# Optimization experiments

Measured on AMD Instinct MI355X. Metric: run time of the kernel, lower is better.

The kernel has to match this reference:

```python
import jax, jax.numpy as jnp
import numpy as np

VAR0, VAR1 = 0.1, 0.2
CONF_THR = 0.02
NMS_THR = 0.4
PRE_K = 5000
POST_K = 750
N = 85680


def setup_inputs() -> dict:
    key = jax.random.key(0)
    k0, k1, k2, k3 = jax.random.split(key, 4)
    return {
        "loc": jax.random.normal(k0, (N, 4), jnp.float32),
        "conf": jax.random.uniform(k1, (N, 2), jnp.float32),
        "landmarks": jax.random.normal(k2, (N, 10), jnp.float32),
        "priors": jax.random.uniform(k3, (N, 4), jnp.float32),
        "img_w": 1920,
        "img_h": 1088,
    }


def _decode_boxes(loc, priors):
    # center-size decode -> xyxy
    cxy = priors[:, :2] + loc[:, :2] * VAR0 * priors[:, 2:]
    wh = priors[:, 2:] * jnp.exp(loc[:, 2:] * VAR1)
    return jnp.concatenate([cxy - wh * 0.5, cxy + wh * 0.5], axis=-1)


def _decode_landmarks(lmk, priors):
    pts = lmk.reshape(-1, 5, 2)                       # [N,5,2]
    out = priors[:, None, :2] + pts * VAR0 * priors[:, None, 2:]
    return out.reshape(-1, 10)


def _pairwise_iou(boxes):
    # boxes: [K,4] xyxy
    area = (boxes[:, 2] - boxes[:, 0]) * (boxes[:, 3] - boxes[:, 1])
    lt = jnp.maximum(boxes[:, None, :2], boxes[None, :, :2])  # [K,K,2]
    rb = jnp.minimum(boxes[:, None, 2:], boxes[None, :, 2:])
    wh = jnp.clip(rb - lt, 0.0)
    inter = wh[..., 0] * wh[..., 1]
    union = area[:, None] + area[None, :] - inter
    return inter / jnp.maximum(union, 1e-12)


def _greedy_nms(boxes, valid, thr):
    # boxes already sorted by descending score; valid marks real candidates.
    K = boxes.shape[0]
    iou = _pairwise_iou(boxes)                         # [K,K]
    idx = jnp.arange(K)

    def body(i, keep):
        suppress = keep[i] & (iou[i] > thr) & (idx > i)
        return keep & ~suppress

    return jax.lax.fori_loop(0, K, body, valid)


def reference(loc, conf, landmarks, priors, img_w, img_h):
    w = jnp.float32(img_w)
    h = jnp.float32(img_h)
    bbox_scale = jnp.array([w, h, w, h], jnp.float32)
    lmk_scale = jnp.tile(jnp.array([w, h], jnp.float32), 5)

    boxes = _decode_boxes(loc, priors) * bbox_scale          # [N,4]
    lmk = _decode_landmarks(landmarks, priors) * lmk_scale   # [N,10]
    scores = conf[:, 1]                                      # [N]

    # confidence filter fused into top-k via -inf masking (static shapes)
    masked = jnp.where(scores > CONF_THR, scores, -jnp.inf)
    top_scores, order = jax.lax.top_k(masked, PRE_K)         # [PRE_K]
    boxes_k = boxes[order]
    lmk_k = lmk[order]
    valid_k = top_scores > CONF_THR

    keep = _greedy_nms(boxes_k, valid_k, NMS_THR)            # [PRE_K] bool

    # compact kept rows (already score-sorted) into fixed [POST_K,15]
    rank = jnp.cumsum(keep) - 1
    rows = jnp.concatenate([boxes_k, top_scores[:, None], lmk_k], axis=1)
    dest = jnp.where(keep & (rank < POST_K), rank, POST_K)   # OOB -> dropped
    out = jnp.zeros((POST_K, 15), jnp.float32).at[dest].set(rows, mode="drop")
    return out
```

## Files before the change

kernel.cpp:

```cpp
#include <hip/hip_runtime.h>
#include <hip/hip_bf16.h>
#include <math.h>

#define N_IN 85680
#define PRE_K 5000
#define POST_K 750
#define NW 79
#define NPAD 5056
#define HSIZE 8192
#define CAND_MAX 8192
#define CONF_THR 0.02f
#define NMS_THR 0.4f
#define BITS_THR 0x3CA3D70Bu
#define NGRP 20
#define ZBYTES 66624

typedef unsigned int u32;
typedef unsigned long long u64;

__device__ __forceinline__ int cbase(int k) { return k * (5088 - 32 * k); }

__device__ __forceinline__ float opaquef(float x) { asm volatile("" : "+v"(x)); return x; }

__device__ __forceinline__ u32 bucket_of(u32 bits) {
    u32 b = (bits - BITS_THR) >> 13;
    return b >= HSIZE ? (HSIZE - 1) : b;
}

__global__ __launch_bounds__(256) void zero_kernel(u32* __restrict__ p) {
    int i = blockIdx.x * 256 + threadIdx.x;
    if (i < ZBYTES / 4) p[i] = 0u;
}

__global__ __launch_bounds__(256) void hist_kernel(const float2* __restrict__ conf2,
                                                   u32* __restrict__ hist) {
    __shared__ u32 h[HSIZE];
    for (int b = threadIdx.x; b < HSIZE; b += 256) h[b] = 0u;
    __syncthreads();
    int i = blockIdx.x * 256 + threadIdx.x;
    if (i < N_IN) {
        float s = conf2[i].y;
        if (s > CONF_THR) atomicAdd(&h[bucket_of(__float_as_uint(s))], 1u);
    }
    __syncthreads();
    for (int b = threadIdx.x; b < HSIZE; b += 256) {
        u32 v = h[b];
        if (v) atomicAdd(&hist[b], v);
    }
}

__global__ __launch_bounds__(1024) void scan_kernel(const u32* __restrict__ hist,
                                                    u32* __restrict__ bsel,
                                                    u32* __restrict__ bstart) {
    __shared__ u32 tot[1024];
    int c = threadIdx.x;
    u32 lh[8];
    u32 t = 0;
#pragma unroll
    for (int k = 0; k < 8; ++k) { lh[k] = hist[c * 8 + k]; t += lh[k]; }
    tot[c] = t;
    __syncthreads();
    for (int d = 1; d < 1024; d <<= 1) {
        u32 v = tot[c] + ((c + d < 1024) ? tot[c + d] : 0u);
        __syncthreads();
        tot[c] = v;
        __syncthreads();
    }
    u32 above = (c + 1 < 1024) ? tot[c + 1] : 0u;
    u32 s = above;
    for (int k = 7; k >= 0; --k) { bstart[c * 8 + k] = s; s += lh[k]; }
    if (above < PRE_K && above + t >= PRE_K) {
        u32 cum = above;
        for (int k = 7; k >= 0; --k) {
            cum += lh[k];
            if (cum >= PRE_K) { bsel[0] = (u32)(c * 8 + k); break; }
        }
    }
    if (c == 0 && tot[0] < PRE_K) bsel[0] = 0u;
}

__global__ __launch_bounds__(256) void compact_kernel(const float2* __restrict__ conf2,
                                                      const u32* __restrict__ bsel,
                                                      const u32* __restrict__ bstart,
                                                      u32* __restrict__ bfill,
                                                      u64* __restrict__ cand) {
    int i = blockIdx.x * 256 + threadIdx.x;
    if (i >= N_IN) return;
    float sc = conf2[i].y;
    if (!(sc > CONF_THR)) return;
    u32 bits = __float_as_uint(sc);
    u32 b = bucket_of(bits);
    if (b < bsel[0]) return;
    u32 pos = bstart[b] + atomicAdd(&bfill[b], 1u);
    if (pos < CAND_MAX) cand[pos] = ((u64)bits << 32) | (u64)(u32)(~(u32)i);
}

__global__ __launch_bounds__(256) void rankdec_kernel(const u64* __restrict__ cand,
                                                      const u32* __restrict__ bstart,
                                                      const u32* __restrict__ bfill,
                                                      const u32* __restrict__ bsel,
                                                      const float4* __restrict__ loc4,
                                                      const float4* __restrict__ pri4,
                                                      const float* __restrict__ lmk,
                                                      const int* __restrict__ imw,
                                                      const int* __restrict__ imh,
                                                      float4* __restrict__ rows4,
                                                      float4* __restrict__ boxes,
                                                      u64* __restrict__ validm) {
    u32 bs = bsel[0];
    u32 total = bstart[bs] + bfill[bs];
    if (total > CAND_MAX) total = CAND_MAX;
    float W = (float)(*imw), H = (float)(*imh);
    for (u32 s = blockIdx.x * blockDim.x + threadIdx.x; s < total;
         s += gridDim.x * blockDim.x) {
        u64 key = cand[s];
        u32 b = bucket_of((u32)(key >> 32));
        u32 st = bstart[b];
        u32 en = st + bfill[b];
        if (en > CAND_MAX) en = CAND_MAX;
        u32 r = st;
        for (u32 j = st; j < en; ++j) r += (cand[j] > key) ? 1u : 0u;
        if (r >= PRE_K) continue;
        u32 i = ~(u32)key;
        float score = __uint_as_float((u32)(key >> 32));
        float4 L = loc4[i];
        float4 P = pri4[i];
        float cx = P.x + opaquef((L.x * 0.1f) * P.z);
        float cy = P.y + opaquef((L.y * 0.1f) * P.w);
        float bw = P.z * (float)exp((double)(L.z * 0.2f));
        float bh = P.w * (float)exp((double)(L.w * 0.2f));
        float hw = opaquef(bw * 0.5f), hh = opaquef(bh * 0.5f);
        float x0 = (cx - hw) * W, y0 = (cy - hh) * H;
        float x1 = (cx + hw) * W, y1 = (cy + hh) * H;
        boxes[r] = make_float4(x0, y0, x1, y1);
        float lm[10];
#pragma unroll
        for (int p = 0; p < 5; ++p) {
            float2 q = ((const float2*)lmk)[(size_t)i * 5 + p];
            lm[2 * p]     = (P.x + opaquef((q.x * 0.1f) * P.z)) * W;
            lm[2 * p + 1] = (P.y + opaquef((q.y * 0.1f) * P.w)) * H;
        }
        float4* row = rows4 + (size_t)r * 4;
        row[0] = make_float4(x0, y0, x1, y1);
        row[1] = make_float4(score, lm[0], lm[1], lm[2]);
        row[2] = make_float4(lm[3], lm[4], lm[5], lm[6]);
        row[3] = make_float4(lm[7], lm[8], lm[9], 0.f);
        atomicOr(&validm[r >> 6], 1ull << (r & 63));
    }
}

__global__ __launch_bounds__(256) void mask_kernel(const float4* __restrict__ boxes,
                                                   u64* __restrict__ cmask) {
    __shared__ float4 cb4[4][64];
    int wv = threadIdx.x >> 6, t = threadIdx.x & 63;
    int t64 = blockIdx.x * 4 + wv;
    if (t64 >= NW * (NW + 1) / 2) return;
    int rc = (int)((sqrtf(8.0f * (float)t64 + 1.0f) - 1.0f) * 0.5f);
    while ((rc + 1) * (rc + 2) / 2 <= t64) ++rc;
    while (rc * (rc + 1) / 2 > t64) --rc;
    int cc = t64 - rc * (rc + 1) / 2;
    cb4[wv][t] = boxes[cc * 64 + t];
    int i = rc * 64 + t;
    float4 bi = boxes[i];
    float areai = (bi.z - bi.x) * (bi.w - bi.y);
    u64 word = 0ull;
#pragma unroll 4
    for (int k = 0; k < 64; ++k) {
        float4 bj = cb4[wv][k];
        float areaj = (bj.z - bj.x) * (bj.w - bj.y);
        float ltx = fmaxf(bi.x, bj.x), lty = fmaxf(bi.y, bj.y);
        float rbx = fminf(bi.z, bj.z), rby = fminf(bi.w, bj.w);
        float wx = fmaxf(rbx - ltx, 0.f), wy = fmaxf(rby - lty, 0.f);
        float inter = opaquef(wx * wy);
        float uni = fmaxf(areai + areaj - inter, 1e-12f);
        float iou = inter / uni;
        if (iou > NMS_THR) word |= (1ull << k);
    }
    if (i < PRE_K) cmask[(size_t)(cbase(cc) + (i - 64 * cc))] = word;
}

#define FC(k, q) cmask[(size_t)(cbase(k) + (q) - 64 * (k))]

#define LDC(j, r, d) ((((d) + (j)) < w0) ? FC((d) + (j), q##r) : 0ull)

#define WAITG(need)                                                                   \
    for (;;) {                                                                        \
        u32 d_ = __hip_atomic_load(&doneCnt, __ATOMIC_RELAXED,                        \
                                   __HIP_MEMORY_SCOPE_WORKGROUP);                     \
        if (d_ > (u32)NGRP) { dead = true; break; }                                   \
        if (d_ >= (u32)(need)) break;                                                 \
    }                                                                                 \
    asm volatile("" ::: "memory");

__device__ __forceinline__ u64 nms_solve(u64 valw, u64 sup, u64 dlow) {
    u64 keep = valw & ~__ballot(sup != 0ull);
    for (;;) {
        u64 conm = __ballot((dlow & keep) != 0ull);
        u64 cm = conm & keep;
        if (cm == 0ull) break;
        u64 U = keep & ~conm;
        u64 rem = __ballot((dlow & U) != 0ull) & keep;
        keep &= ~rem;
    }
    return keep;
}

__global__ __launch_bounds__(512) void reduce_scatter_kernel(const u64* __restrict__ cmask,
                                                             const u64* __restrict__ validm,
                                                             const float* __restrict__ rows,
                                                             float* __restrict__ out) {
    int tid = threadIdx.x;
    int g = tid >> 6, lane = tid & 63;
    __shared__ u64 keepAll[96];
    __shared__ u32 totG[32];
    __shared__ u32 doneCnt;
    __shared__ u32 wpref[97];
    for (int k = tid; k < 96; k += 512) keepAll[k] = 0ull;
    if (tid == 0) doneCnt = 0u;
    __syncthreads();
    u64 lmask = (1ull << lane) - 1ull;

    for (int s = 0; s < 3; ++s) {
        int G = s * 8 + g;
        if (G >= NGRP) break;
        int w0 = 4 * G;
        int nwg = NW - w0; if (nwg > 4) nwg = 4;
        int q0 = 64 * w0 + lane;
        int q1 = q0 + 64;
        int q2 = q0 + 128;
        int q3 = (nwg > 3) ? (q0 + 192) : q0;
        u64 t00 = FC(w0, q0);
        u64 t10 = (nwg > 1) ? FC(w0, q1) : 0ull;
        u64 t11 = (nwg > 1) ? FC(w0 + 1, q1) : 0ull;
        u64 t20 = (nwg > 2) ? FC(w0, q2) : 0ull;
        u64 t21 = (nwg > 2) ? FC(w0 + 1, q2) : 0ull;
        u64 t22 = (nwg > 2) ? FC(w0 + 2, q2) : 0ull;
        u64 t30 = (nwg > 3) ? FC(w0, q3) : 0ull;
        u64 t31 = (nwg > 3) ? FC(w0 + 1, q3) : 0ull;
        u64 t32 = (nwg > 3) ? FC(w0 + 2, q3) : 0ull;
        u64 t33 = (nwg > 3) ? FC(w0 + 3, q3) : 0ull;
        u64 v0 = validm[w0];
        u64 v1 = (nwg > 1) ? validm[w0 + 1] : 0ull;
        u64 v2 = (nwg > 2) ? validm[w0 + 2] : 0ull;
        u64 v3 = (nwg > 3) ? validm[w0 + 3] : 0ull;
        u64 sup0 = 0, sup1 = 0, sup2 = 0, sup3 = 0;
        bool dead = false;

        int d0 = 0;
        u64 a00=0,a01=0,a02=0,a03=0, a10=0,a11=0,a12=0,a13=0,
            a20=0,a21=0,a22=0,a23=0, a30=0,a31=0,a32=0,a33=0;
        if (w0 > 0) {
            a00=LDC(0,0,0); a01=LDC(0,1,0); a02=LDC(0,2,0); a03=LDC(0,3,0);
            a10=LDC(1,0,0); a11=LDC(1,1,0); a12=LDC(1,2,0); a13=LDC(1,3,0);
            a20=LDC(2,0,0); a21=LDC(2,1,0); a22=LDC(2,2,0); a23=LDC(2,3,0);
            a30=LDC(3,0,0); a31=LDC(3,1,0); a32=LDC(3,2,0); a33=LDC(3,3,0);
        }
        asm volatile("" ::: "memory");
        while (d0 < w0) {
            int d1 = d0 + 4;
            u64 b00=0,b01=0,b02=0,b03=0, b10=0,b11=0,b12=0,b13=0,
                b20=0,b21=0,b22=0,b23=0, b30=0,b31=0,b32=0,b33=0;
            if (d1 < w0) {
                b00=LDC(0,0,d1); b01=LDC(0,1,d1); b02=LDC(0,2,d1); b03=LDC(0,3,d1);
                b10=LDC(1,0,d1); b11=LDC(1,1,d1); b12=LDC(1,2,d1); b13=LDC(1,3,d1);
                b20=LDC(2,0,d1); b21=LDC(2,1,d1); b22=LDC(2,2,d1); b23=LDC(2,3,d1);
                b30=LDC(3,0,d1); b31=LDC(3,1,d1); b32=LDC(3,2,d1); b33=LDC(3,3,d1);
            }
            asm volatile("" ::: "memory");
            WAITG((d0 >> 2) + 1)
            if (dead) break;
            u64 ka = keepAll[d0],     kb = keepAll[d0 + 1];
            u64 kc = keepAll[d0 + 2], kd = keepAll[d0 + 3];
            sup0 |= ((ka & a00) | (kb & a10)) | ((kc & a20) | (kd & a30));
            sup1 |= ((ka & a01) | (kb & a11)) | ((kc & a21) | (kd & a31));
            sup2 |= ((ka & a02) | (kb & a12)) | ((kc & a22) | (kd & a32));
            sup3 |= ((ka & a03) | (kb & a13)) | ((kc & a23) | (kd & a33));
            a00=b00;a01=b01;a02=b02;a03=b03; a10=b10;a11=b11;a12=b12;a13=b13;
            a20=b20;a21=b21;a22=b22;a23=b23; a30=b30;a31=b31;a32=b32;a33=b33;
            d0 = d1;
        }
        if (!dead) {
            __builtin_amdgcn_s_setprio(1);
            u32 tp = (G > 0) ? totG[G - 1] : 0u;
            u64 k0 = 0, k1 = 0, k2 = 0, k3 = 0;
            if (tp < POST_K) {
                k0 = nms_solve(v0, sup0, t00 & lmask);
                sup1 |= k0 & t10; sup2 |= k0 & t20; sup3 |= k0 & t30;
                k1 = nms_solve(v1, sup1, t11 & lmask);
                sup2 |= k1 & t21; sup3 |= k1 & t31;
                k2 = nms_solve(v2, sup2, t22 & lmask);
                sup3 |= k2 & t32;
                k3 = nms_solve(v3, sup3, t33 & lmask);
            }
            if (lane == 0) {
                keepAll[w0]     = k0;
                keepAll[w0 + 1] = k1;
                keepAll[w0 + 2] = k2;
                keepAll[w0 + 3] = k3;
                u32 tk = tp + (u32)(__popcll(k0) + __popcll(k1) + __popcll(k2) + __popcll(k3));
                totG[G] = tk;
                asm volatile("s_waitcnt lgkmcnt(0)" ::: "memory");
                __hip_atomic_store(&doneCnt,
                                   (tk >= POST_K) ? (u32)(NGRP + 9) : (u32)(G + 1),
                                   __ATOMIC_RELAXED, __HIP_MEMORY_SCOPE_WORKGROUP);
            }
            __builtin_amdgcn_s_setprio(0);
        } else {
            break;
        }
    }
    __syncthreads();

    if (tid == 0) {
        u32 s = 0;
        for (int w = 0; w < NW; ++w) { wpref[w] = s; s += (u32)__popcll(keepAll[w]); }
        wpref[NW] = s;
    }
    __syncthreads();
    u32 totk = wpref[NW]; if (totk > POST_K) totk = POST_K;
    for (int r = tid; r < PRE_K; r += 512) {
        int w = r >> 6, b = r & 63;
        u64 kw = keepAll[w];
        if ((kw >> b) & 1ull) {
            u32 rank = wpref[w] + (u32)__popcll(kw & ((1ull << b) - 1ull));
            if (rank < POST_K) {
                const float* src = rows + (size_t)r * 16;
                float* dst = out + (size_t)rank * 15;
#pragma unroll
                for (int c2 = 0; c2 < 15; ++c2) dst[c2] = src[c2];
            }
        }
    }
    for (int r = (int)totk + tid; r < POST_K; r += 512) {
        float* dst = out + (size_t)r * 15;
#pragma unroll
        for (int c2 = 0; c2 < 15; ++c2) dst[c2] = 0.f;
    }
}

extern "C" void kernel_launch(void* const* d_in, const int* in_sizes, int n_in,
                              void* d_out, int out_size, void* d_ws, size_t ws_size,
                              hipStream_t stream) {
    const float* loc = (const float*)d_in[0];
    const float2* conf2 = (const float2*)d_in[1];
    const float* lmk = (const float*)d_in[2];
    const float* pri = (const float*)d_in[3];
    const int* imw = (const int*)d_in[4];
    const int* imh = (const int*)d_in[5];
    float* out = (float*)d_out;
    char* base = (char*)d_ws;

    u32* hist   = (u32*)(base + 0);
    u32* bfill  = (u32*)(base + 32768);
    u32* bsel   = (u32*)(base + 65536);
    u64* validm = (u64*)(base + 65600);
    u32* bstart = (u32*)(base + 67648);
    u64* cand   = (u64*)(base + 100416);
    float* rows = (float*)(base + 165952);
    float4* boxes = (float4*)(base + 485952);
    u64* cmask  = (u64*)(base + 566848);

    zero_kernel<<<(ZBYTES / 4 + 255) / 256, 256, 0, stream>>>((u32*)base);

    hist_kernel<<<(N_IN + 255) / 256, 256, 0, stream>>>(conf2, hist);
    scan_kernel<<<1, 1024, 0, stream>>>(hist, bsel, bstart);
    compact_kernel<<<(N_IN + 255) / 256, 256, 0, stream>>>(conf2, bsel, bstart, bfill, cand);
    rankdec_kernel<<<48, 256, 0, stream>>>(cand, bstart, bfill, bsel, (const float4*)loc,
                                           (const float4*)pri, lmk, imw, imh,
                                           (float4*)rows, boxes, validm);
    mask_kernel<<<(NW * (NW + 1) / 2 + 3) / 4, 256, 0, stream>>>(boxes, cmask);
    reduce_scatter_kernel<<<1, 512, 0, stream>>>(cmask, validm, rows, out);
}
```

Before: 93.44 us.

## Fuse histogram scan and candidate compaction into one kernel with a spin-wait flag

The single-block scan kernel and the compaction kernel are merged into one launch. Block 0 computes the bucket prefix sums and threshold bucket over 256 threads with 32 buckets each, then publishes a release flag. The other blocks preload their scores and spin on an acquire load until the flag is set. This removes one kernel launch boundary and overlaps the score loads with the scan. The cost is spin-waiting blocks and reliance on block 0 being scheduled, which is a forward-progress assumption.

```diff
diff --git a/kernel.cpp b/kernel.cpp
--- a/kernel.cpp
+++ b/kernel.cpp
@@ -49,45 +49,54 @@
     }
 }
 
-__global__ __launch_bounds__(1024) void scan_kernel(const u32* __restrict__ hist,
-                                                    u32* __restrict__ bsel,
-                                                    u32* __restrict__ bstart) {
-    __shared__ u32 tot[1024];
+__global__ __launch_bounds__(256) void scancompact_kernel(const float2* __restrict__ conf2,
+                                                          const u32* __restrict__ hist,
+                                                          u32* __restrict__ bsel,
+                                                          u32* __restrict__ bstart,
+                                                          u32* __restrict__ bfill,
+                                                          u32* __restrict__ flag,
+                                                          u64* __restrict__ cand) {
     int c = threadIdx.x;
-    u32 lh[8];
-    u32 t = 0;
-#pragma unroll
-    for (int k = 0; k < 8; ++k) { lh[k] = hist[c * 8 + k]; t += lh[k]; }
-    tot[c] = t;
-    __syncthreads();
-    for (int d = 1; d < 1024; d <<= 1) {
-        u32 v = tot[c] + ((c + d < 1024) ? tot[c + d] : 0u);
+    if (blockIdx.x == 0) {
+        __shared__ u32 tot[256];
+        u32 lh[32];
+        u32 t = 0;
+#pragma unroll
+        for (int k = 0; k < 32; ++k) { lh[k] = hist[c * 32 + k]; t += lh[k]; }
+        tot[c] = t;
         __syncthreads();
-        tot[c] = v;
+        for (int d = 1; d < 256; d <<= 1) {
+            u32 v = tot[c] + ((c + d < 256) ? tot[c + d] : 0u);
+            __syncthreads();
+            tot[c] = v;
+            __syncthreads();
+        }
+        u32 above = (c + 1 < 256) ? tot[c + 1] : 0u;
+        u32 s = above;
+#pragma unroll
+        for (int k = 31; k >= 0; --k) { bstart[c * 32 + k] = s; s += lh[k]; }
+        if (above < PRE_K && above + t >= PRE_K) {
+            u32 cum = above;
+#pragma unroll
+            for (int k = 31; k >= 0; --k) {
+                cum += lh[k];
+                if (cum >= PRE_K) { bsel[0] = (u32)(c * 32 + k); break; }
+            }
+        }
+        if (c == 0 && tot[0] < PRE_K) bsel[0] = 0u;
         __syncthreads();
-    }
-    u32 above = (c + 1 < 1024) ? tot[c + 1] : 0u;
-    u32 s = above;
-    for (int k = 7; k >= 0; --k) { bstart[c * 8 + k] = s; s += lh[k]; }
-    if (above < PRE_K && above + t >= PRE_K) {
-        u32 cum = above;
-        for (int k = 7; k >= 0; --k) {
-            cum += lh[k];
-            if (cum >= PRE_K) { bsel[0] = (u32)(c * 8 + k); break; }
-        }
-    }
-    if (c == 0 && tot[0] < PRE_K) bsel[0] = 0u;
-}
-
-__global__ __launch_bounds__(256) void compact_kernel(const float2* __restrict__ conf2,
-                                                      const u32* __restrict__ bsel,
-                                                      const u32* __restrict__ bstart,
-                                                      u32* __restrict__ bfill,
-                                                      u64* __restrict__ cand) {
-    int i = blockIdx.x * 256 + threadIdx.x;
-    if (i >= N_IN) return;
-    float sc = conf2[i].y;
-    if (!(sc > CONF_THR)) return;
+        if (c == 0)
+            __hip_atomic_store(flag, 1u, __ATOMIC_RELEASE, __HIP_MEMORY_SCOPE_AGENT);
+        return;
+    }
+    int i = (blockIdx.x - 1) * 256 + c;
+    float sc = (i < N_IN) ? conf2[i].y : 0.f;
+    asm volatile("" ::: "memory");
+    for (;;) {
+        if (__hip_atomic_load(flag, __ATOMIC_ACQUIRE, __HIP_MEMORY_SCOPE_AGENT)) break;
+        __builtin_amdgcn_s_sleep(8);
+    }
+    if (i >= N_IN || !(sc > CONF_THR)) return;
     u32 bits = __float_as_uint(sc);
     u32 b = bucket_of(bits);
     if (b < bsel[0]) return;
@@ -353,6 +362,7 @@
     u32* hist   = (u32*)(base + 0);
     u32* bfill  = (u32*)(base + 32768);
     u32* bsel   = (u32*)(base + 65536);
+    u32* flag   = (u32*)(base + 65540);
     u64* validm = (u64*)(base + 65600);
     u32* bstart = (u32*)(base + 67648);
     u64* cand   = (u64*)(base + 100416);
@@ -363,8 +373,8 @@
     zero_kernel<<<(ZBYTES / 4 + 255) / 256, 256, 0, stream>>>((u32*)base);
 
     hist_kernel<<<(N_IN + 255) / 256, 256, 0, stream>>>(conf2, hist);
-    scan_kernel<<<1, 1024, 0, stream>>>(hist, bsel, bstart);
-    compact_kernel<<<(N_IN + 255) / 256, 256, 0, stream>>>(conf2, bsel, bstart, bfill, cand);
+    scancompact_kernel<<<1 + (N_IN + 255) / 256, 256, 0, stream>>>(conf2, hist, bsel,
+                                                                   bstart, bfill, flag, cand);
     rankdec_kernel<<<48, 256, 0, stream>>>(cand, bstart, bfill, bsel, (const float4*)loc,
                                            (const float4*)pri, lmk, imw, imh,
                                            (float4*)rows, boxes, validm);
```

Result: slower. 144.7 us (+54.9%).
